# Performance work log

Measured on AMD Instinct MI355X. Metric: run time of the kernel, lower is better.

## Reference

```python
import jax, jax.numpy as jnp
import numpy as np

B, L, D, H = 2, 2048, 1024, 16
HD = D // H
SCALE = HD ** -0.5


def setup_inputs() -> dict:
    key = jax.random.key(0)
    ks = jax.random.split(key, 11)
    s = D ** -0.5  # torch Linear default init scale (uniform bound)
    return {
        "q": jax.random.normal(ks[0], (B, L, D), jnp.float32),
        "k": jax.random.normal(ks[1], (B, L, D), jnp.float32),
        "v": jax.random.normal(ks[2], (B, L, D), jnp.float32),
        "Wq": jax.random.uniform(ks[3], (D, D), jnp.float32, -s, s),
        "bq": jax.random.uniform(ks[4], (D,), jnp.float32, -s, s),
        "Wk": jax.random.uniform(ks[5], (D, D), jnp.float32, -s, s),
        "bk": jax.random.uniform(ks[6], (D,), jnp.float32, -s, s),
        "Wv": jax.random.uniform(ks[7], (D, D), jnp.float32, -s, s),
        "bv": jax.random.uniform(ks[8], (D,), jnp.float32, -s, s),
        "Wo": jax.random.uniform(ks[9], (D, D), jnp.float32, -s, s),
        "bo": jax.random.uniform(ks[10], (D,), jnp.float32, -s, s),
    }


def reference(q, k, v, Wq, bq, Wk, bk, Wv, bv, Wo, bo):
    b, q_len, _ = q.shape
    # projections; weights stored as (D, D) acting on the right: x @ W + b
    qh = (q @ Wq + bq).reshape(b, q_len, H, HD).transpose(0, 2, 1, 3)  # (B,H,Q,hd)
    kh = (k @ Wk + bk).reshape(b, -1, H, HD).transpose(0, 2, 1, 3)    # (B,H,K,hd)
    vh = (v @ Wv + bv).reshape(b, -1, H, HD).transpose(0, 2, 1, 3)    # (B,H,K,hd)
    att = jnp.einsum("bhqd,bhkd->bhqk", qh * SCALE, kh)               # (B,H,Q,K)
    att = jax.nn.softmax(att, axis=-1)
    out = jnp.einsum("bhqk,bhkd->bhqd", att, vh)                      # (B,H,Q,hd)
    out = out.transpose(0, 2, 1, 3).reshape(b, q_len, D)
    return out @ Wo + bo
```

## Files before the change

### kernel.cpp

```cpp
#include <hip/hip_runtime.h>

namespace {
constexpr int kB  = 2;
constexpr int kL  = 2048;
constexpr int kD  = 1024;
constexpr int kH  = 16;
constexpr int kHD = 64;
constexpr int kM  = kB * kL;
}

typedef _Float16 f16x8 __attribute__((ext_vector_type(8)));
typedef float    f32x16 __attribute__((ext_vector_type(16)));
typedef unsigned int u32;

union Frag16 { uint4 u4; unsigned u[4]; f16x8 v; };

__device__ __forceinline__ unsigned short f2h(float f) {
    return __builtin_bit_cast(unsigned short, (_Float16)f);
}
__device__ __forceinline__ unsigned pk2(float a, float b) {
    return __builtin_bit_cast(unsigned, __builtin_amdgcn_cvt_pkrtz(a, b));
}

__device__ __forceinline__ void gload16(const void* g, void* l) {
    __builtin_amdgcn_global_load_lds(
        (const __attribute__((address_space(1))) u32*)g,
        (__attribute__((address_space(3))) u32*)(unsigned long long)(__builtin_bit_cast(unsigned long long, l)),
        16, 0, 0);
}

__global__ __launch_bounds__(256) void cast_f16_kernel(
    const float* __restrict__ q, const float* __restrict__ k,
    const float* __restrict__ v, unsigned short* __restrict__ dst)
{
    const float* src = blockIdx.y == 0 ? q : (blockIdx.y == 1 ? k : v);
    unsigned short* d = dst + (size_t)blockIdx.y * ((size_t)kM * kD);
    const size_t i = ((size_t)blockIdx.x * 256 + threadIdx.x) * 8;
    const float4 f0 = *(const float4*)(src + i);
    const float4 f1 = *(const float4*)(src + i + 4);
    _Float16 h[8];
    h[0] = (_Float16)f0.x; h[1] = (_Float16)f0.y;
    h[2] = (_Float16)f0.z; h[3] = (_Float16)f0.w;
    h[4] = (_Float16)f1.x; h[5] = (_Float16)f1.y;
    h[6] = (_Float16)f1.z; h[7] = (_Float16)f1.w;
    *(uint4*)(d + i) = *(uint4*)h;
}

__global__ __launch_bounds__(256) void tcast_kernel(
    const float* __restrict__ W0, const float* __restrict__ W1,
    const float* __restrict__ W2, const float* __restrict__ W3,
    unsigned short* __restrict__ WtBase)
{
    __shared__ _Float16 T[64][68];
    const float* W = blockIdx.z == 0 ? W0 : blockIdx.z == 1 ? W1
                   : blockIdx.z == 2 ? W2 : W3;
    unsigned short* Wt = WtBase + (size_t)blockIdx.z * ((size_t)kD * kD);
    const int k0 = blockIdx.y * 64, n0 = blockIdx.x * 64;
    const int tx = threadIdx.x & 15, ty = threadIdx.x >> 4;
#pragma unroll
    for (int i = 0; i < 4; ++i) {
        const int kk = i * 16 + ty;
        const float4 w = *(const float4*)&W[(size_t)(k0 + kk) * kD + n0 + tx * 4];
        T[tx * 4 + 0][kk] = (_Float16)w.x;
        T[tx * 4 + 1][kk] = (_Float16)w.y;
        T[tx * 4 + 2][kk] = (_Float16)w.z;
        T[tx * 4 + 3][kk] = (_Float16)w.w;
    }
    __syncthreads();
#pragma unroll
    for (int i = 0; i < 4; ++i) {
        const int nn = i * 16 + ty;
        *(ushort4*)&Wt[(size_t)(n0 + nn) * kD + k0 + tx * 4] = *(ushort4*)&T[nn][tx * 4];
    }
}

__global__ __launch_bounds__(256) void gemm_qkv_kernel(
    const unsigned short* __restrict__ A, const unsigned short* __restrict__ Wt,
    const float* __restrict__ bq, const float* __restrict__ bk,
    const float* __restrict__ bv, unsigned short* __restrict__ Qh,
    unsigned short* __restrict__ Kh, unsigned short* __restrict__ Vt)
{
    __shared__ unsigned short Als[2][128 * 64];
    __shared__ unsigned short Bls[2][128 * 64];

    const int tid = threadIdx.x;
    const int lane = tid & 63;
    const int wid = tid >> 6;
    const int l31 = lane & 31;
    const int hi = lane >> 5;
    const int by = blockIdx.x & 31;
    const int bxp = blockIdx.x >> 5;
    const int proj = bxp >> 3;
    const int bx = bxp & 7;
    const int row0 = by * 128;
    const int col0 = bx * 128;
    const int wr = wid >> 1, wc = wid & 1;

    const int rl = lane >> 3;
    const int sl = lane & 7;
    const int ssrc = (sl ^ rl) * 8;

    const unsigned short* Aproj = A + (size_t)proj * ((size_t)kM * kD);
    const unsigned short* Wproj = Wt + (size_t)proj * ((size_t)kD * kD);
    const unsigned short* Abase = Aproj + (size_t)(row0 + wid * 32 + rl) * kD + ssrc;
    const unsigned short* Bbase = Wproj + (size_t)(col0 + wid * 32 + rl) * kD + ssrc;

    f32x16 acc00{}, acc01{}, acc10{}, acc11{};

    auto stage = [&](int kt, int buf) {
#pragma unroll
        for (int i = 0; i < 4; ++i) {
            gload16(Abase + (size_t)(i * 8) * kD + kt * 64,
                    &Als[buf][(wid * 32 + i * 8) * 64]);
        }
#pragma unroll
        for (int i = 0; i < 4; ++i) {
            gload16(Bbase + (size_t)(i * 8) * kD + kt * 64,
                    &Bls[buf][(wid * 32 + i * 8) * 64]);
        }
    };

    const int ra0 = wr * 64 + l31;
    const int cb0 = wc * 64 + l31;

    stage(0, 0);
    int cur = 0;
    for (int kt = 0; kt < kD / 64; ++kt) {
        __syncthreads();
        if (kt + 1 < kD / 64) stage(kt + 1, cur ^ 1);
#pragma unroll
        for (int ks = 0; ks < 4; ++ks) {
            const int slot = (ks << 1) | hi;
            Frag16 a0, a1, b0, b1;
            a0.u4 = *(const uint4*)&Als[cur][ra0 * 64 + ((slot ^ (ra0 & 7)) << 3)];
            a1.u4 = *(const uint4*)&Als[cur][(ra0 + 32) * 64 + ((slot ^ ((ra0 + 32) & 7)) << 3)];
            b0.u4 = *(const uint4*)&Bls[cur][cb0 * 64 + ((slot ^ (cb0 & 7)) << 3)];
            b1.u4 = *(const uint4*)&Bls[cur][(cb0 + 32) * 64 + ((slot ^ ((cb0 + 32) & 7)) << 3)];
            acc00 = __builtin_amdgcn_mfma_f32_32x32x16_f16(a0.v, b0.v, acc00, 0, 0, 0);
            acc01 = __builtin_amdgcn_mfma_f32_32x32x16_f16(a0.v, b1.v, acc01, 0, 0, 0);
            acc10 = __builtin_amdgcn_mfma_f32_32x32x16_f16(a1.v, b0.v, acc10, 0, 0, 0);
            acc11 = __builtin_amdgcn_mfma_f32_32x32x16_f16(a1.v, b1.v, acc11, 0, 0, 0);
        }
        cur ^= 1;
    }

    const float* bias = proj == 0 ? bq : (proj == 1 ? bk : bv);
    const float bias0 = bias[col0 + wc * 64 + l31];
    const float bias1 = bias[col0 + wc * 64 + 32 + l31];

    const f32x16* accs[2][2] = {{&acc00, &acc01}, {&acc10, &acc11}};
#pragma unroll
    for (int rt = 0; rt < 2; ++rt) {
#pragma unroll
        for (int ct = 0; ct < 2; ++ct) {
            const f32x16& acv = *accs[rt][ct];
            const float bb = ct ? bias1 : bias0;
            const int c = col0 + wc * 64 + ct * 32 + l31;
            if (proj == 2) {
#pragma unroll
                for (int qd = 0; qd < 4; ++qd) {
                    const int r = row0 + wr * 64 + rt * 32 + 8 * qd + 4 * hi;
                    const int b_ = r >> 11, l_ = r & (kL - 1);
                    ushort4 w;
                    w.x = f2h(acv[4 * qd + 0] + bb);
                    w.y = f2h(acv[4 * qd + 1] + bb);
                    w.z = f2h(acv[4 * qd + 2] + bb);
                    w.w = f2h(acv[4 * qd + 3] + bb);
                    *(ushort4*)&Vt[((size_t)(b_ * kH + (c >> 6)) * kHD + (c & 63)) * kL + l_] = w;
                }
            } else {
                unsigned short* C = proj == 0 ? Qh : Kh;
#pragma unroll
                for (int reg = 0; reg < 16; ++reg) {
                    const int r = row0 + wr * 64 + rt * 32 + (reg & 3) + 8 * (reg >> 2) + 4 * hi;
                    const int b_ = r >> 11, l_ = r & (kL - 1);
                    C[((size_t)(b_ * kH + (c >> 6)) * kL + l_) * kHD + (c & 63)] = f2h(acv[reg] + bb);
                }
            }
        }
    }
}

__global__ __launch_bounds__(256) void gemm_o_kernel(
    const unsigned short* __restrict__ A, const unsigned short* __restrict__ Wt,
    const float* __restrict__ bias, float* __restrict__ C)
{
    __shared__ unsigned short Als[2][128 * 64];
    __shared__ unsigned short Bls[2][64 * 64];

    const int tid = threadIdx.x;
    const int lane = tid & 63;
    const int wid = tid >> 6;
    const int l31 = lane & 31;
    const int hi = lane >> 5;
    const int by = blockIdx.x & 31;
    const int bx = blockIdx.x >> 5;
    const int row0 = by * 128;
    const int wr = wid >> 1, wc = wid & 1;

    const int rl = lane >> 3;
    const int sl = lane & 7;
    const int ssrc = (sl ^ rl) * 8;

    const unsigned short* Abase = A + (size_t)(row0 + wid * 32 + rl) * kD + ssrc;
    const unsigned short* Bbase = Wt + (size_t)(bx * 64 + wid * 16 + rl) * kD + ssrc;

    f32x16 acc0{}, acc1{};

    auto stage = [&](int kt, int buf) {
#pragma unroll
        for (int i = 0; i < 4; ++i)
            gload16(Abase + (size_t)(i * 8) * kD + kt * 64,
                    &Als[buf][(wid * 32 + i * 8) * 64]);
        gload16(Bbase + kt * 64,                   &Bls[buf][(wid * 16) * 64]);
        gload16(Bbase + (size_t)8 * kD + kt * 64,  &Bls[buf][(wid * 16 + 8) * 64]);
    };

    const int ra0 = wr * 64 + l31;
    const int cb0 = wc * 32 + l31;

    stage(0, 0);
    int cur = 0;
    for (int kt = 0; kt < kD / 64; ++kt) {
        __syncthreads();
        if (kt + 1 < kD / 64) stage(kt + 1, cur ^ 1);
#pragma unroll
        for (int ks = 0; ks < 4; ++ks) {
            const int slot = (ks << 1) | hi;
            Frag16 a0, a1, b0;
            a0.u4 = *(const uint4*)&Als[cur][ra0 * 64 + ((slot ^ (ra0 & 7)) << 3)];
            a1.u4 = *(const uint4*)&Als[cur][(ra0 + 32) * 64 + ((slot ^ ((ra0 + 32) & 7)) << 3)];
            b0.u4 = *(const uint4*)&Bls[cur][cb0 * 64 + ((slot ^ (cb0 & 7)) << 3)];
            acc0 = __builtin_amdgcn_mfma_f32_32x32x16_f16(a0.v, b0.v, acc0, 0, 0, 0);
            acc1 = __builtin_amdgcn_mfma_f32_32x32x16_f16(a1.v, b0.v, acc1, 0, 0, 0);
        }
        cur ^= 1;
    }

    const int c = (bx << 6) + wc * 32 + l31;
    const float bb = bias[c];
    const f32x16* accs[2] = {&acc0, &acc1};
#pragma unroll
    for (int rt = 0; rt < 2; ++rt) {
        const f32x16& acv = *accs[rt];
#pragma unroll
        for (int reg = 0; reg < 16; ++reg) {
            const int r = row0 + wr * 64 + rt * 32 + (reg & 3) + 8 * (reg >> 2) + 4 * hi;
            C[(size_t)r * kD + c] = acv[reg] + bb;
        }
    }
}

__global__ __launch_bounds__(512) void attn_mfma_kernel(
    const unsigned short* __restrict__ Qh, const unsigned short* __restrict__ Kh,
    const unsigned short* __restrict__ Vt, unsigned short* __restrict__ Opart,
    float2* __restrict__ Stat)
{
    __shared__ unsigned short Kls[4][64 * 64];
    __shared__ unsigned short Vls[4][64 * 64];

    const int lane = threadIdx.x & 63;
    const int wid  = threadIdx.x >> 6;
    const int l31  = lane & 31;
    const int hi   = lane >> 5;

    const int id = blockIdx.x;
    const int j  = id >> 3;
    const int bh = (id & 7) * 4 + (j >> 4);
    const int qt = j & 7;
    const int ks = (j >> 3) & 1;
    const int q = qt * 256 + wid * 32 + l31;

    const size_t qkBase = (size_t)bh * kL * kHD;
    const unsigned short* Qp = Qh + qkBase + (size_t)q * kHD + hi * 8;
    Frag16 qf[4];
#pragma unroll
    for (int d = 0; d < 4; ++d) qf[d].u4 = *(const uint4*)(Qp + d * 16);

    const int srow = wid * 8 + (lane >> 3);
    const int soff = (((lane & 7) ^ (srow & 7)) << 3);
    const unsigned short* Kg = Kh + qkBase + (size_t)srow * kHD + soff;
    const unsigned short* Vg = Vt + (size_t)bh * kHD * kL + (size_t)srow * kL + soff;

    auto stage = [&](int kt, int buf) {
        gload16(Kg + (size_t)(kt * 64) * kHD, &Kls[buf][(wid * 8) * 64]);
        gload16(Vg + kt * 64,                 &Vls[buf][(wid * 8) * 64]);
    };

    auto buildpf = [&](const unsigned* u, Frag16* pf) {
        unsigned t0 = hi ? u[0] : u[2];
        unsigned t1 = hi ? u[1] : u[3];
        unsigned t2 = hi ? u[4] : u[6];
        unsigned t3 = hi ? u[5] : u[7];
        const unsigned r0 = __shfl_xor(t0, 32);
        const unsigned r1 = __shfl_xor(t1, 32);
        const unsigned r2 = __shfl_xor(t2, 32);
        const unsigned r3 = __shfl_xor(t3, 32);
        pf[0].u[0] = hi ? r0 : u[0];
        pf[0].u[1] = hi ? r1 : u[1];
        pf[0].u[2] = hi ? u[2] : r0;
        pf[0].u[3] = hi ? u[3] : r1;
        pf[1].u[0] = hi ? r2 : u[4];
        pf[1].u[1] = hi ? r3 : u[5];
        pf[1].u[2] = hi ? u[6] : r2;
        pf[1].u[3] = hi ? u[7] : r3;
    };

    f32x16 o0{}, o1{};
    float lsum = 0.f;
    const float cexp = 0.125f * 1.44269504089f;
    const int rA = l31, rB = l31 + 32;

    const int kt0 = ks * 16;
    stage(kt0 + 0, 0);
    stage(kt0 + 1, 1);

    for (int rt = 0; rt < 8; ++rt) {
        const int t0 = 2 * rt;
        asm volatile("s_waitcnt vmcnt(0)" ::: "memory");
        __builtin_amdgcn_s_barrier();
        if (t0 + 3 < 16) {
            stage(kt0 + t0 + 2, (t0 + 2) & 3);
            stage(kt0 + t0 + 3, (t0 + 3) & 3);
        }
        const int bA = t0 & 3, bB = (t0 + 1) & 3;

        f32x16 c0{}, c1{}, c2{}, c3{};
        __builtin_amdgcn_s_setprio(1);
#pragma unroll
        for (int d = 0; d < 4; ++d) {
            const int s = (d << 1) | hi;
            Frag16 ka0, ka1, kb0, kb1;
            ka0.u4 = *(const uint4*)&Kls[bA][rA * 64 + ((s ^ (rA & 7)) << 3)];
            ka1.u4 = *(const uint4*)&Kls[bA][rB * 64 + ((s ^ (rB & 7)) << 3)];
            kb0.u4 = *(const uint4*)&Kls[bB][rA * 64 + ((s ^ (rA & 7)) << 3)];
            kb1.u4 = *(const uint4*)&Kls[bB][rB * 64 + ((s ^ (rB & 7)) << 3)];
            c0 = __builtin_amdgcn_mfma_f32_32x32x16_f16(ka0.v, qf[d].v, c0, 0, 0, 0);
            c1 = __builtin_amdgcn_mfma_f32_32x32x16_f16(ka1.v, qf[d].v, c1, 0, 0, 0);
            c2 = __builtin_amdgcn_mfma_f32_32x32x16_f16(kb0.v, qf[d].v, c2, 0, 0, 0);
            c3 = __builtin_amdgcn_mfma_f32_32x32x16_f16(kb1.v, qf[d].v, c3, 0, 0, 0);
        }
        __builtin_amdgcn_s_setprio(0);

        float rs = 0.f;
        unsigned uA0[8], uA1[8], uB0[8], uB1[8];
#pragma unroll
        for (int i = 0; i < 8; ++i) {
            const float e0 = __builtin_amdgcn_exp2f(c0[2 * i] * cexp);
            const float e1 = __builtin_amdgcn_exp2f(c0[2 * i + 1] * cexp);
            const float e2 = __builtin_amdgcn_exp2f(c1[2 * i] * cexp);
            const float e3 = __builtin_amdgcn_exp2f(c1[2 * i + 1] * cexp);
            const float e4 = __builtin_amdgcn_exp2f(c2[2 * i] * cexp);
            const float e5 = __builtin_amdgcn_exp2f(c2[2 * i + 1] * cexp);
            const float e6 = __builtin_amdgcn_exp2f(c3[2 * i] * cexp);
            const float e7 = __builtin_amdgcn_exp2f(c3[2 * i + 1] * cexp);
            uA0[i] = pk2(e0, e1);
            uA1[i] = pk2(e2, e3);
            uB0[i] = pk2(e4, e5);
            uB1[i] = pk2(e6, e7);
            rs += ((e0 + e1) + (e2 + e3)) + ((e4 + e5) + (e6 + e7));
        }
        rs += __shfl_xor(rs, 32);
        lsum += rs;

        {
            Frag16 pf[4];
            buildpf(uA0, &pf[0]);
            buildpf(uA1, &pf[2]);
            __builtin_amdgcn_s_setprio(1);
#pragma unroll
            for (int ksl = 0; ksl < 4; ++ksl) {
                const int s = (ksl << 1) | hi;
                Frag16 v0, v1;
                v0.u4 = *(const uint4*)&Vls[bA][rA * 64 + ((s ^ (rA & 7)) << 3)];
                v1.u4 = *(const uint4*)&Vls[bA][rB * 64 + ((s ^ (rB & 7)) << 3)];
                o0 = __builtin_amdgcn_mfma_f32_32x32x16_f16(v0.v, pf[ksl].v, o0, 0, 0, 0);
                o1 = __builtin_amdgcn_mfma_f32_32x32x16_f16(v1.v, pf[ksl].v, o1, 0, 0, 0);
            }
            __builtin_amdgcn_s_setprio(0);
        }
        {
            Frag16 pf[4];
            buildpf(uB0, &pf[0]);
            buildpf(uB1, &pf[2]);
            __builtin_amdgcn_s_setprio(1);
#pragma unroll
            for (int ksl = 0; ksl < 4; ++ksl) {
                const int s = (ksl << 1) | hi;
                Frag16 v0, v1;
                v0.u4 = *(const uint4*)&Vls[bB][rA * 64 + ((s ^ (rA & 7)) << 3)];
                v1.u4 = *(const uint4*)&Vls[bB][rB * 64 + ((s ^ (rB & 7)) << 3)];
                o0 = __builtin_amdgcn_mfma_f32_32x32x16_f16(v0.v, pf[ksl].v, o0, 0, 0, 0);
                o1 = __builtin_amdgcn_mfma_f32_32x32x16_f16(v1.v, pf[ksl].v, o1, 0, 0, 0);
            }
            __builtin_amdgcn_s_setprio(0);
        }
    }

    const size_t prow = (size_t)ks * (32 * kL) + (size_t)bh * kL + q;
    const float inv = 1.f / lsum;
    unsigned short* pp = Opart + prow * kHD;
#pragma unroll
    for (int g = 0; g < 4; ++g) {
        const int d = g * 8 + hi * 4;
        uint2 w0, w1;
        w0.x = pk2(o0[4 * g + 0] * inv, o0[4 * g + 1] * inv);
        w0.y = pk2(o0[4 * g + 2] * inv, o0[4 * g + 3] * inv);
        w1.x = pk2(o1[4 * g + 0] * inv, o1[4 * g + 1] * inv);
        w1.y = pk2(o1[4 * g + 2] * inv, o1[4 * g + 3] * inv);
        *(uint2*)(pp + d) = w0;
        *(uint2*)(pp + 32 + d) = w1;
    }
    if (hi == 0) Stat[prow] = make_float2(0.f, lsum);
}

__global__ __launch_bounds__(256) void merge_kernel(
    const unsigned short* __restrict__ Opart, const float2* __restrict__ Stat,
    unsigned short* __restrict__ O16)
{
    const int g = blockIdx.x * 256 + threadIdx.x;
    const int row = g >> 3;
    const int d0 = (g & 7) * 8;
    const int bh = row >> 11, q = row & (kL - 1);
    const float2 sa = Stat[row];
    const float2 sb = Stat[32 * kL + row];
    const float cexp = 0.125f * 1.44269504089f;
    const float M = fmaxf(sa.x, sb.x);
    float wa = __builtin_amdgcn_exp2f((sa.x - M) * cexp) * sa.y;
    float wb = __builtin_amdgcn_exp2f((sb.x - M) * cexp) * sb.y;
    const float inv = 1.f / (wa + wb);
    wa *= inv; wb *= inv;

    const unsigned short* pa = Opart + (size_t)row * kHD + d0;
    const unsigned short* pb = pa + (size_t)32 * kL * kHD;
    uint4 ua = *(const uint4*)pa;
    uint4 ub = *(const uint4*)pb;
    _Float16 ha[8], hb[8];
    *(uint4*)ha = ua;
    *(uint4*)hb = ub;
    unsigned out[4];
#pragma unroll
    for (int i = 0; i < 4; ++i) {
        const float v0 = wa * (float)ha[2 * i]     + wb * (float)hb[2 * i];
        const float v1 = wa * (float)ha[2 * i + 1] + wb * (float)hb[2 * i + 1];
        out[i] = pk2(v0, v1);
    }
    const int b_ = bh >> 4, h_ = bh & 15;
    *(uint4*)&O16[((size_t)(b_ * kL + q)) * kD + h_ * kHD + d0] = *(uint4*)out;
}

extern "C" void kernel_launch(void* const* d_in, const int* in_sizes, int n_in,
                              void* d_out, int out_size, void* d_ws, size_t ws_size,
                              hipStream_t stream)
{
    const float* q  = (const float*)d_in[0];
    const float* k  = (const float*)d_in[1];
    const float* v  = (const float*)d_in[2];
    const float* Wq = (const float*)d_in[3];
    const float* bq = (const float*)d_in[4];
    const float* Wk = (const float*)d_in[5];
    const float* bk = (const float*)d_in[6];
    const float* Wv = (const float*)d_in[7];
    const float* bv = (const float*)d_in[8];
    const float* Wo = (const float*)d_in[9];
    const float* bo = (const float*)d_in[10];
    float* out = (float*)d_out;

    const size_t MD = (size_t)kM * kD;
    const size_t DD = (size_t)kD * kD;
    unsigned short* A16 = (unsigned short*)d_ws;
    unsigned short* Wt16 = A16 + 3 * MD;
    unsigned short* Qh16 = Wt16 + 4 * DD;
    unsigned short* Kh16 = Qh16 + MD;
    unsigned short* Vt16 = Kh16 + MD;
    unsigned short* O16   = A16;
    unsigned short* Opart = A16 + MD;
    float2*         Stat  = (float2*)Wt16;

    const dim3 blk(256);

    hipLaunchKernelGGL(cast_f16_kernel, dim3(kM * kD / (256 * 8), 3), blk, 0, stream,
                       q, k, v, A16);
    hipLaunchKernelGGL(tcast_kernel, dim3(16, 16, 4), blk, 0, stream,
                       Wq, Wk, Wv, Wo, Wt16);

    hipLaunchKernelGGL(gemm_qkv_kernel, dim3(32 * 24), blk, 0, stream,
                       A16, Wt16, bq, bk, bv, Qh16, Kh16, Vt16);

    hipLaunchKernelGGL(attn_mfma_kernel, dim3(512), dim3(512), 0, stream,
                       Qh16, Kh16, Vt16, Opart, Stat);
    hipLaunchKernelGGL(merge_kernel, dim3(2048), blk, 0, stream,
                       Opart, Stat, O16);

    hipLaunchKernelGGL(gemm_o_kernel, dim3(32 * 16), blk, 0, stream,
                       O16, Wt16 + 3 * DD, bo, out);
}
```

Before: 131.3 us.

## Fuse cast kernels, fold softmax scale into Q, drop P-fragment shuffles

Merges the activation cast and the weight transpose-cast into one launch, removing a kernel launch boundary. Folds the softmax scale and log2e factor into the Q projection epilogue, so the attention loop skips a multiply per score. Permutes the V-transpose store order within each 16-token group (the row index is XOR-swizzled), so the exp'd P values can be packed straight into MFMA operand fragments without cross-lane shuffles. Also simplifies the merge weights, since the max is always zero. These ideas change numerics slightly and depend on the swizzle matching the MFMA lane layout exactly.

```diff
diff --git a/kernel.cpp b/kernel.cpp
--- a/kernel.cpp
+++ b/kernel.cpp
@@ -29,33 +29,38 @@
         16, 0, 0);
 }
 
-__global__ __launch_bounds__(256) void cast_f16_kernel(
+__global__ __launch_bounds__(256) void prep_kernel(
     const float* __restrict__ q, const float* __restrict__ k,
-    const float* __restrict__ v, unsigned short* __restrict__ dst)
-{
-    const float* src = blockIdx.y == 0 ? q : (blockIdx.y == 1 ? k : v);
-    unsigned short* d = dst + (size_t)blockIdx.y * ((size_t)kM * kD);
-    const size_t i = ((size_t)blockIdx.x * 256 + threadIdx.x) * 8;
-    const float4 f0 = *(const float4*)(src + i);
-    const float4 f1 = *(const float4*)(src + i + 4);
-    _Float16 h[8];
-    h[0] = (_Float16)f0.x; h[1] = (_Float16)f0.y;
-    h[2] = (_Float16)f0.z; h[3] = (_Float16)f0.w;
-    h[4] = (_Float16)f1.x; h[5] = (_Float16)f1.y;
-    h[6] = (_Float16)f1.z; h[7] = (_Float16)f1.w;
-    *(uint4*)(d + i) = *(uint4*)h;
-}
-
-__global__ __launch_bounds__(256) void tcast_kernel(
+    const float* __restrict__ v, unsigned short* __restrict__ dstA,
     const float* __restrict__ W0, const float* __restrict__ W1,
     const float* __restrict__ W2, const float* __restrict__ W3,
     unsigned short* __restrict__ WtBase)
 {
     __shared__ _Float16 T[64][68];
-    const float* W = blockIdx.z == 0 ? W0 : blockIdx.z == 1 ? W1
-                   : blockIdx.z == 2 ? W2 : W3;
-    unsigned short* Wt = WtBase + (size_t)blockIdx.z * ((size_t)kD * kD);
-    const int k0 = blockIdx.y * 64, n0 = blockIdx.x * 64;
+    const int id = blockIdx.x;
+    if (id < 6144) {
+        const int yy = id >> 11;
+        const int xx = id & 2047;
+        const float* src = yy == 0 ? q : (yy == 1 ? k : v);
+        unsigned short* d = dstA + (size_t)yy * ((size_t)kM * kD);
+        const size_t i = ((size_t)xx * 256 + threadIdx.x) * 8;
+        const float4 f0 = *(const float4*)(src + i);
+        const float4 f1 = *(const float4*)(src + i + 4);
+        _Float16 h[8];
+        h[0] = (_Float16)f0.x; h[1] = (_Float16)f0.y;
+        h[2] = (_Float16)f0.z; h[3] = (_Float16)f0.w;
+        h[4] = (_Float16)f1.x; h[5] = (_Float16)f1.y;
+        h[6] = (_Float16)f1.z; h[7] = (_Float16)f1.w;
+        *(uint4*)(d + i) = *(uint4*)h;
+        return;
+    }
+    const int id2 = id - 6144;
+    const int z = id2 >> 8;
+    const int rem = id2 & 255;
+    const int by = rem >> 4, bx = rem & 15;
+    const float* W = z == 0 ? W0 : z == 1 ? W1 : z == 2 ? W2 : W3;
+    unsigned short* Wt = WtBase + (size_t)z * ((size_t)kD * kD);
+    const int k0 = by * 64, n0 = bx * 64;
     const int tx = threadIdx.x & 15, ty = threadIdx.x >> 4;
 #pragma unroll
     for (int i = 0; i < 4; ++i) {
@@ -147,6 +152,7 @@
     const float* bias = proj == 0 ? bq : (proj == 1 ? bk : bv);
     const float bias0 = bias[col0 + wc * 64 + l31];
     const float bias1 = bias[col0 + wc * 64 + 32 + l31];
+    const float oscale = proj == 0 ? (0.125f * 1.44269504089f) : 1.0f;
 
     const f32x16* accs[2][2] = {{&acc00, &acc01}, {&acc10, &acc11}};
 #pragma unroll
@@ -160,7 +166,9 @@
 #pragma unroll
                 for (int qd = 0; qd < 4; ++qd) {
                     const int r = row0 + wr * 64 + rt * 32 + 8 * qd + 4 * hi;
-                    const int b_ = r >> 11, l_ = r & (kL - 1);
+                    const int b_ = r >> 11;
+                    int l_ = r & (kL - 1);
+                    l_ ^= ((((l_ >> 2) ^ (l_ >> 3)) & 1) ? 12 : 0);
                     ushort4 w;
                     w.x = f2h(acv[4 * qd + 0] + bb);
                     w.y = f2h(acv[4 * qd + 1] + bb);
@@ -174,7 +182,8 @@
                 for (int reg = 0; reg < 16; ++reg) {
                     const int r = row0 + wr * 64 + rt * 32 + (reg & 3) + 8 * (reg >> 2) + 4 * hi;
                     const int b_ = r >> 11, l_ = r & (kL - 1);
-                    C[((size_t)(b_ * kH + (c >> 6)) * kL + l_) * kHD + (c & 63)] = f2h(acv[reg] + bb);
+                    C[((size_t)(b_ * kH + (c >> 6)) * kL + l_) * kHD + (c & 63)] =
+                        f2h((acv[reg] + bb) * oscale);
                 }
             }
         }
@@ -287,28 +296,8 @@
         gload16(Vg + kt * 64,                 &Vls[buf][(wid * 8) * 64]);
     };
 
-    auto buildpf = [&](const unsigned* u, Frag16* pf) {
-        unsigned t0 = hi ? u[0] : u[2];
-        unsigned t1 = hi ? u[1] : u[3];
-        unsigned t2 = hi ? u[4] : u[6];
-        unsigned t3 = hi ? u[5] : u[7];
-        const unsigned r0 = __shfl_xor(t0, 32);
-        const unsigned r1 = __shfl_xor(t1, 32);
-        const unsigned r2 = __shfl_xor(t2, 32);
-        const unsigned r3 = __shfl_xor(t3, 32);
-        pf[0].u[0] = hi ? r0 : u[0];
-        pf[0].u[1] = hi ? r1 : u[1];
-        pf[0].u[2] = hi ? u[2] : r0;
-        pf[0].u[3] = hi ? u[3] : r1;
-        pf[1].u[0] = hi ? r2 : u[4];
-        pf[1].u[1] = hi ? r3 : u[5];
-        pf[1].u[2] = hi ? u[6] : r2;
-        pf[1].u[3] = hi ? u[7] : r3;
-    };
-
     f32x16 o0{}, o1{};
     float lsum = 0.f;
-    const float cexp = 0.125f * 1.44269504089f;
     const int rA = l31, rB = l31 + 32;
 
     const int kt0 = ks * 16;
@@ -343,58 +332,46 @@
         __builtin_amdgcn_s_setprio(0);
 
         float rs = 0.f;
-        unsigned uA0[8], uA1[8], uB0[8], uB1[8];
+        Frag16 pfA[4], pfB[4];
 #pragma unroll
         for (int i = 0; i < 8; ++i) {
-            const float e0 = __builtin_amdgcn_exp2f(c0[2 * i] * cexp);
-            const float e1 = __builtin_amdgcn_exp2f(c0[2 * i + 1] * cexp);
-            const float e2 = __builtin_amdgcn_exp2f(c1[2 * i] * cexp);
-            const float e3 = __builtin_amdgcn_exp2f(c1[2 * i + 1] * cexp);
-            const float e4 = __builtin_amdgcn_exp2f(c2[2 * i] * cexp);
-            const float e5 = __builtin_amdgcn_exp2f(c2[2 * i + 1] * cexp);
-            const float e6 = __builtin_amdgcn_exp2f(c3[2 * i] * cexp);
-            const float e7 = __builtin_amdgcn_exp2f(c3[2 * i + 1] * cexp);
-            uA0[i] = pk2(e0, e1);
-            uA1[i] = pk2(e2, e3);
-            uB0[i] = pk2(e4, e5);
-            uB1[i] = pk2(e6, e7);
+            const float e0 = __builtin_amdgcn_exp2f(c0[2 * i]);
+            const float e1 = __builtin_amdgcn_exp2f(c0[2 * i + 1]);
+            const float e2 = __builtin_amdgcn_exp2f(c1[2 * i]);
+            const float e3 = __builtin_amdgcn_exp2f(c1[2 * i + 1]);
+            const float e4 = __builtin_amdgcn_exp2f(c2[2 * i]);
+            const float e5 = __builtin_amdgcn_exp2f(c2[2 * i + 1]);
+            const float e6 = __builtin_amdgcn_exp2f(c3[2 * i]);
+            const float e7 = __builtin_amdgcn_exp2f(c3[2 * i + 1]);
+            pfA[i >> 2].u[i & 3]       = pk2(e0, e1);
+            pfA[2 + (i >> 2)].u[i & 3] = pk2(e2, e3);
+            pfB[i >> 2].u[i & 3]       = pk2(e4, e5);
+            pfB[2 + (i >> 2)].u[i & 3] = pk2(e6, e7);
             rs += ((e0 + e1) + (e2 + e3)) + ((e4 + e5) + (e6 + e7));
         }
         rs += __shfl_xor(rs, 32);
         lsum += rs;
 
-        {
-            Frag16 pf[4];
-            buildpf(uA0, &pf[0]);
-            buildpf(uA1, &pf[2]);
-            __builtin_amdgcn_s_setprio(1);
-#pragma unroll
-            for (int ksl = 0; ksl < 4; ++ksl) {
-                const int s = (ksl << 1) | hi;
-                Frag16 v0, v1;
-                v0.u4 = *(const uint4*)&Vls[bA][rA * 64 + ((s ^ (rA & 7)) << 3)];
-                v1.u4 = *(const uint4*)&Vls[bA][rB * 64 + ((s ^ (rB & 7)) << 3)];
-                o0 = __builtin_amdgcn_mfma_f32_32x32x16_f16(v0.v, pf[ksl].v, o0, 0, 0, 0);
-                o1 = __builtin_amdgcn_mfma_f32_32x32x16_f16(v1.v, pf[ksl].v, o1, 0, 0, 0);
-            }
-            __builtin_amdgcn_s_setprio(0);
-        }
-        {
-            Frag16 pf[4];
-            buildpf(uB0, &pf[0]);
-            buildpf(uB1, &pf[2]);
-            __builtin_amdgcn_s_setprio(1);
-#pragma unroll
-            for (int ksl = 0; ksl < 4; ++ksl) {
-                const int s = (ksl << 1) | hi;
-                Frag16 v0, v1;
-                v0.u4 = *(const uint4*)&Vls[bB][rA * 64 + ((s ^ (rA & 7)) << 3)];
-                v1.u4 = *(const uint4*)&Vls[bB][rB * 64 + ((s ^ (rB & 7)) << 3)];
-                o0 = __builtin_amdgcn_mfma_f32_32x32x16_f16(v0.v, pf[ksl].v, o0, 0, 0, 0);
-                o1 = __builtin_amdgcn_mfma_f32_32x32x16_f16(v1.v, pf[ksl].v, o1, 0, 0, 0);
-            }
-            __builtin_amdgcn_s_setprio(0);
-        }
+        __builtin_amdgcn_s_setprio(1);
+#pragma unroll
+        for (int ksl = 0; ksl < 4; ++ksl) {
+            const int s = (ksl << 1) | hi;
+            Frag16 v0, v1;
+            v0.u4 = *(const uint4*)&Vls[bA][rA * 64 + ((s ^ (rA & 7)) << 3)];
+            v1.u4 = *(const uint4*)&Vls[bA][rB * 64 + ((s ^ (rB & 7)) << 3)];
+            o0 = __builtin_amdgcn_mfma_f32_32x32x16_f16(v0.v, pfA[ksl].v, o0, 0, 0, 0);
+            o1 = __builtin_amdgcn_mfma_f32_32x32x16_f16(v1.v, pfA[ksl].v, o1, 0, 0, 0);
+        }
+#pragma unroll
+        for (int ksl = 0; ksl < 4; ++ksl) {
+            const int s = (ksl << 1) | hi;
+            Frag16 v0, v1;
+            v0.u4 = *(const uint4*)&Vls[bB][rA * 64 + ((s ^ (rA & 7)) << 3)];
+            v1.u4 = *(const uint4*)&Vls[bB][rB * 64 + ((s ^ (rB & 7)) << 3)];
+            o0 = __builtin_amdgcn_mfma_f32_32x32x16_f16(v0.v, pfB[ksl].v, o0, 0, 0, 0);
+            o1 = __builtin_amdgcn_mfma_f32_32x32x16_f16(v1.v, pfB[ksl].v, o1, 0, 0, 0);
+        }
+        __builtin_amdgcn_s_setprio(0);
     }
 
     const size_t prow = (size_t)ks * (32 * kL) + (size_t)bh * kL + q;
@@ -424,10 +401,8 @@
     const int bh = row >> 11, q = row & (kL - 1);
     const float2 sa = Stat[row];
     const float2 sb = Stat[32 * kL + row];
-    const float cexp = 0.125f * 1.44269504089f;
-    const float M = fmaxf(sa.x, sb.x);
-    float wa = __builtin_amdgcn_exp2f((sa.x - M) * cexp) * sa.y;
-    float wb = __builtin_amdgcn_exp2f((sb.x - M) * cexp) * sb.y;
+    float wa = sa.y;
+    float wb = sb.y;
     const float inv = 1.f / (wa + wb);
     wa *= inv; wb *= inv;
 
@@ -479,10 +454,8 @@
 
     const dim3 blk(256);
 
-    hipLaunchKernelGGL(cast_f16_kernel, dim3(kM * kD / (256 * 8), 3), blk, 0, stream,
-                       q, k, v, A16);
-    hipLaunchKernelGGL(tcast_kernel, dim3(16, 16, 4), blk, 0, stream,
-                       Wq, Wk, Wv, Wo, Wt16);
+    hipLaunchKernelGGL(prep_kernel, dim3(7168), blk, 0, stream,
+                       q, k, v, A16, Wq, Wk, Wv, Wo, Wt16);
 
     hipLaunchKernelGGL(gemm_qkv_kernel, dim3(32 * 24), blk, 0, stream,
                        A16, Wt16, bq, bk, bv, Qh16, Kh16, Vt16);
```

Result: faster. 123.0 us (-6.3%).
